# Kernel tuning notes

Hardware: AMD Instinct MI355X
Metric: run time of the kernel (lower is better)

The kernel has to match this reference:

```python
import jax, jax.numpy as jnp
import numpy as np

B, N, D, H = 8, 1024, 512, 512  # batch, nodes/graph, input dim, hidden/output dim
NEG_SLOPE = 0.2


def _gatv2_layer(x, src, dst, Wl, bl, Wr, br, a, bias, nseg):
    """PyG GATv2Conv (heads=1, add_self_loops=False, eval mode -> no dropout).
    message j->i: alpha_ij = softmax_i( a . leaky_relu(xl[j] + xr[i]) ); out[i] = sum_j alpha_ij * xl[j] + bias
    """
    xl = x @ Wl + bl              # [nseg, H] source transform
    xr = x @ Wr + br              # [nseg, H] target transform
    e = jax.nn.leaky_relu(xl[src] + xr[dst], NEG_SLOPE) @ a  # [E] raw scores
    m = jax.lax.stop_gradient(jax.ops.segment_max(e, dst, num_segments=nseg))
    ex = jnp.exp(e - m[dst])
    s = jax.ops.segment_sum(ex, dst, num_segments=nseg)
    alpha = ex / s[dst]                                       # segment softmax over incoming edges
    out = jax.ops.segment_sum(alpha[:, None] * xl[src], dst, num_segments=nseg)
    return out + bias


def setup_inputs() -> dict:
    key = jax.random.key(0)
    rng = np.random.RandomState(0)
    # random per-graph adjacency, avg degree ~16; block-diagonal edge extraction
    adj_np = (rng.rand(B, N, N) < (16.0 / N))
    srcs, dsts = [], []
    for b in range(B):  # matches torch.nonzero(big_adj).t(): row=src, col=dst
        r, c = np.nonzero(adj_np[b])
        srcs.append(r + b * N)
        dsts.append(c + b * N)
    edge_index = jnp.asarray(np.stack([np.concatenate(srcs), np.concatenate(dsts)]).astype(np.int32))

    ks = jax.random.split(key, 32)
    def lin(k, fi, fo):
        return (jax.random.normal(k, (fi, fo), jnp.float32) / np.sqrt(fi)).astype(jnp.float32)
    inp = {
        "batch_graph": jax.random.normal(ks[0], (B, N, D), jnp.float32),
        "adj": jnp.asarray(adj_np.astype(np.float32)),
        "edge_index": edge_index,
    }
    dims = [(D, H), (H, H), (H, H)]
    for i, (fi, fo) in enumerate(dims, start=1):
        k = jax.random.split(ks[i], 6)
        inp[f"Wl{i}"] = lin(k[0], fi, fo)
        inp[f"bl{i}"] = jnp.zeros((fo,), jnp.float32)
        inp[f"Wr{i}"] = lin(k[1], fi, fo)
        inp[f"br{i}"] = jnp.zeros((fo,), jnp.float32)
        inp[f"a{i}"] = (jax.random.normal(k[2], (fo,), jnp.float32) / np.sqrt(fo)).astype(jnp.float32)
        inp[f"bias{i}"] = jnp.zeros((fo,), jnp.float32)
    return inp


def reference(batch_graph, adj, edge_index,
              Wl1, bl1, Wr1, br1, a1, bias1,
              Wl2, bl2, Wr2, br2, a2, bias2,
              Wl3, bl3, Wr3, br3, a3, bias3):
    b, n, d = batch_graph.shape
    nseg = b * n
    x = batch_graph.reshape(nseg, d)
    src, dst = edge_index[0], edge_index[1]
    x = _gatv2_layer(x, src, dst, Wl1, bl1, Wr1, br1, a1, bias1, nseg)  # graph_norm = Identity
    x = _gatv2_layer(x, src, dst, Wl2, bl2, Wr2, br2, a2, bias2, nseg)
    x = _gatv2_layer(x, src, dst, Wl3, bl3, Wr3, br3, a3, bias3, nseg)
    return x.reshape(b, n, -1)
```

## Files before the change

kernel.cpp:

```cpp
#include <hip/hip_runtime.h>
#include <math.h>

#define MTOT 8192
#define HD   512

typedef __attribute__((ext_vector_type(8))) short bf16x8;
typedef __attribute__((ext_vector_type(4))) float floatx4;

__device__ inline unsigned short f2bf(float f) {
    unsigned int u = __float_as_uint(f);
    unsigned int r = (u + 0x7FFFu + ((u >> 16) & 1u)) >> 16;
    return (unsigned short)r;
}
__device__ inline float bf2f(unsigned short h) {
    return __uint_as_float(((unsigned int)h) << 16);
}


__global__ void count_deg(const int* __restrict__ dst, int* __restrict__ deg, int E) {
    int i = blockIdx.x * 256 + threadIdx.x;
    if (i < E) atomicAdd(&deg[dst[i]], 1);
}

__global__ __launch_bounds__(1024) void scan_offsets(const int* __restrict__ deg,
                                                     int* __restrict__ offs,
                                                     int* __restrict__ cursor) {
    __shared__ int part[1024];
    int tid = threadIdx.x;
    int base = tid * 8;
    int v[8]; int s = 0;
    #pragma unroll
    for (int i = 0; i < 8; ++i) { v[i] = deg[base + i]; s += v[i]; }
    part[tid] = s;
    __syncthreads();
    for (int off = 1; off < 1024; off <<= 1) {
        int t = (tid >= off) ? part[tid - off] : 0;
        __syncthreads();
        part[tid] += t;
        __syncthreads();
    }
    int run = (tid == 0) ? 0 : part[tid - 1];
    #pragma unroll
    for (int i = 0; i < 8; ++i) {
        offs[base + i] = run;
        cursor[base + i] = run;
        run += v[i];
    }
    if (tid == 1023) offs[MTOT] = run;
}

__global__ void scatter_edges(const int* __restrict__ src, const int* __restrict__ dst,
                              int* __restrict__ cursor, int* __restrict__ csr_src, int E) {
    int i = blockIdx.x * 256 + threadIdx.x;
    if (i < E) {
        int p = atomicAdd(&cursor[dst[i]], 1);
        csr_src[p] = src[i];
    }
}


__global__ __launch_bounds__(256) void prep_convert(
    const float* __restrict__ W0, const float* __restrict__ W1,
    const float* __restrict__ W2, const float* __restrict__ W3,
    const float* __restrict__ W4, const float* __restrict__ W5,
    unsigned short* __restrict__ wtbase,
    const float* __restrict__ X,
    unsigned short* __restrict__ Ahi, unsigned short* __restrict__ Alo,
    int* __restrict__ deg)
{
    int z = blockIdx.z;
    if (z == 7) {
        if (blockIdx.x == 0 && blockIdx.y == 0)
            for (int i = threadIdx.x; i < MTOT; i += 256) deg[i] = 0;
        return;
    }
    if (z == 6) {
        int bid = blockIdx.x * 16 + blockIdx.y;
        int t0 = bid * 256 + threadIdx.x;
        #pragma unroll
        for (int it = 0; it < 16; ++it) {
            int i = (t0 + it * 65536) * 4;
            float4 vv = *(const float4*)(X + i);
            ushort4 h, l;
            h.x = f2bf(vv.x); l.x = f2bf(vv.x - bf2f(h.x));
            h.y = f2bf(vv.y); l.y = f2bf(vv.y - bf2f(h.y));
            h.z = f2bf(vv.z); l.z = f2bf(vv.z - bf2f(h.z));
            h.w = f2bf(vv.w); l.w = f2bf(vv.w - bf2f(h.w));
            *(ushort4*)(Ahi + i) = h;
            *(ushort4*)(Alo + i) = l;
        }
        return;
    }
    const float* W = (z == 0) ? W0 : (z == 1) ? W1 : (z == 2) ? W2
                   : (z == 3) ? W3 : (z == 4) ? W4 : W5;
    int L = z >> 1, lr = z & 1;
    const size_t SZ = (size_t)HD * HD;
    unsigned short* Whi = wtbase + (L * 4 + lr * 2) * SZ;
    unsigned short* Wlo = Whi + SZ;

    __shared__ float t[32][33];
    int bx = blockIdx.x * 32;
    int by = blockIdx.y * 32;
    int tx = threadIdx.x & 31, ty = threadIdx.x >> 5;
    for (int i = ty; i < 32; i += 8)
        t[i][tx] = W[(size_t)(by + i) * HD + bx + tx];
    __syncthreads();
    for (int i = ty; i < 32; i += 8) {
        float vv = t[tx][i];
        unsigned short h = f2bf(vv);
        unsigned short l = f2bf(vv - bf2f(h));
        Whi[(size_t)(bx + i) * HD + by + tx] = h;
        Wlo[(size_t)(bx + i) * HD + by + tx] = l;
    }
}


__global__ __launch_bounds__(256) void gemm_mfma_dual(
    const unsigned short* __restrict__ Ahi, const unsigned short* __restrict__ Alo,
    const unsigned short* __restrict__ Bhi_l, const unsigned short* __restrict__ Blo_l,
    const unsigned short* __restrict__ Bhi_r, const unsigned short* __restrict__ Blo_r,
    const float* __restrict__ bias_l, const float* __restrict__ bias_r,
    float* __restrict__ Cl, float* __restrict__ Cr)
{
    const unsigned short* Bhi = blockIdx.z ? Bhi_r : Bhi_l;
    const unsigned short* Blo = blockIdx.z ? Blo_r : Blo_l;
    const float* bias         = blockIdx.z ? bias_r : bias_l;
    float* C                  = blockIdx.z ? Cr : Cl;

    __shared__ __align__(16) unsigned short lds[4 * 128 * 32];

    int tid = threadIdx.x;
    int wave = tid >> 6, lane = tid & 63;
    int bm = blockIdx.y * 128, bn = blockIdx.x * 128;

    const unsigned short* gsrc[4] = {Ahi, Alo, Bhi, Blo};
    int rowbase[4] = {bm, bm, bn, bn};

    const unsigned short* gbase =
        gsrc[wave] + (size_t)(rowbase[wave] + (lane >> 2)) * 512 + (lane & 3) * 8;

    floatx4 acc[4][4] = {};

    int wm = wave & 1, wn = wave >> 1;
    int lr = lane & 15, lq = lane >> 4;

    for (int k0 = 0; k0 < 512; k0 += 32) {
        const unsigned short* g = gbase + k0;
        #pragma unroll
        for (int rg = 0; rg < 8; ++rg) {
            __builtin_amdgcn_global_load_lds(
                (const __attribute__((address_space(1))) unsigned int*)(g + (size_t)rg * 16 * 512),
                (__attribute__((address_space(3))) unsigned int*)(&lds[wave * 4096 + rg * 512]),
                16, 0, 0);
        }
        __syncthreads();

        bf16x8 ah[4], al[4], bh[4], bl_[4];
        #pragma unroll
        for (int i = 0; i < 4; ++i) {
            int mrow = wm * 64 + i * 16 + lr;
            ah[i]  = *(const bf16x8*)&lds[0 * 4096 + mrow * 32 + lq * 8];
            al[i]  = *(const bf16x8*)&lds[1 * 4096 + mrow * 32 + lq * 8];
            int nrow = wn * 64 + i * 16 + lr;
            bh[i]  = *(const bf16x8*)&lds[2 * 4096 + nrow * 32 + lq * 8];
            bl_[i] = *(const bf16x8*)&lds[3 * 4096 + nrow * 32 + lq * 8];
        }
        #pragma unroll
        for (int i = 0; i < 4; ++i)
            #pragma unroll
            for (int j = 0; j < 4; ++j) {
                acc[i][j] = __builtin_amdgcn_mfma_f32_16x16x32_bf16(ah[i], bh[j],  acc[i][j], 0, 0, 0);
                acc[i][j] = __builtin_amdgcn_mfma_f32_16x16x32_bf16(ah[i], bl_[j], acc[i][j], 0, 0, 0);
                acc[i][j] = __builtin_amdgcn_mfma_f32_16x16x32_bf16(al[i], bh[j],  acc[i][j], 0, 0, 0);
            }
        __syncthreads();
    }

    #pragma unroll
    for (int j = 0; j < 4; ++j) {
        int n = bn + wn * 64 + j * 16 + lr;
        float bv = bias[n];
        #pragma unroll
        for (int i = 0; i < 4; ++i) {
            int mbase = bm + wm * 64 + i * 16 + lq * 4;
            #pragma unroll
            for (int r = 0; r < 4; ++r)
                C[(size_t)(mbase + r) * 512 + n] = acc[i][j][r] + bv;
        }
    }
}


__global__ __launch_bounds__(512) void gat_fused3(
    const float* __restrict__ xl, const float* __restrict__ xr,
    const float* __restrict__ avec, const float* __restrict__ bias,
    const int* __restrict__ offs, const int* __restrict__ csr_src,
    float* __restrict__ out, unsigned short* __restrict__ Ohi,
    unsigned short* __restrict__ Olo, int write_fp32)
{
    __shared__ float xr_sh[4][512];
    __shared__ float sc_sh[4][128];
    __shared__ int   idx_sh[4][128];
    __shared__ float inv_sh[4];

    int gid = blockIdx.x;
    int nbase = ((gid & 7) << 10) + ((gid >> 3) << 2);
    int tid = threadIdx.x;
    int wv = tid >> 6, lane = tid & 63;

    int o0 = offs[nbase], o1 = offs[nbase + 1], o2 = offs[nbase + 2];
    int o3 = offs[nbase + 3], o4 = offs[nbase + 4];

    {
        int row = tid >> 7, col = tid & 127;
        *(float4*)&xr_sh[row][col * 4] =
            *(const float4*)(xr + (size_t)(nbase + row) * HD + col * 4);
    }
    if (wv < 4) {
        int nb = (wv == 0) ? o0 : (wv == 1) ? o1 : (wv == 2) ? o2 : o3;
        int ne = (wv == 0) ? o1 : (wv == 1) ? o2 : (wv == 2) ? o3 : o4;
        int dg = ne - nb; if (dg > 128) dg = 128;
        for (int i = lane; i < dg; i += 64) idx_sh[wv][i] = csr_src[nb + i];
    }
    __syncthreads();

    {
        int sub = lane >> 4, flane = lane & 15;
        float4 av[8];
        #pragma unroll
        for (int i = 0; i < 8; ++i)
            av[i] = *(const float4*)(avec + i * 64 + flane * 4);

        for (int p0 = o0 + wv * 4; p0 < o4; p0 += 32) {
            int p = p0 + sub;
            bool valid = p < o4;
            int pc = valid ? p : o0;
            int nid = (pc >= o1) + (pc >= o2) + (pc >= o3);
            int nb = (nid == 0) ? o0 : (nid == 1) ? o1 : (nid == 2) ? o2 : o3;
            int local = pc - nb;
            valid = valid && (local < 128);
            int j = idx_sh[nid][valid ? local : 0];
            const float* xls = xl + (size_t)j * HD;
            float pe0 = 0.f, pe1 = 0.f;
            #pragma unroll
            for (int i = 0; i < 8; ++i) {
                float4 xv = *(const float4*)(xls + i * 64 + flane * 4);
                float4 rv = *(const float4*)&xr_sh[nid][i * 64 + flane * 4];
                float t;
                t = xv.x + rv.x; pe0 = fmaf(av[i].x, t, pe0); pe1 = fmaf(av[i].x, fabsf(t), pe1);
                t = xv.y + rv.y; pe0 = fmaf(av[i].y, t, pe0); pe1 = fmaf(av[i].y, fabsf(t), pe1);
                t = xv.z + rv.z; pe0 = fmaf(av[i].z, t, pe0); pe1 = fmaf(av[i].z, fabsf(t), pe1);
                t = xv.w + rv.w; pe0 = fmaf(av[i].w, t, pe0); pe1 = fmaf(av[i].w, fabsf(t), pe1);
            }
            float pe = fmaf(0.6f, pe0, 0.4f * pe1);
            pe += __shfl_xor(pe, 1, 64);
            pe += __shfl_xor(pe, 2, 64);
            pe += __shfl_xor(pe, 4, 64);
            pe += __shfl_xor(pe, 8, 64);
            if (valid && flane == 0) sc_sh[nid][local] = pe;
        }
    }
    __syncthreads();

    if (wv < 4) {
        int nb = (wv == 0) ? o0 : (wv == 1) ? o1 : (wv == 2) ? o2 : o3;
        int ne = (wv == 0) ? o1 : (wv == 1) ? o2 : (wv == 2) ? o3 : o4;
        int dg = ne - nb; if (dg > 128) dg = 128;
        float s0v = (lane < dg) ? sc_sh[wv][lane] : -1e30f;
        float s1v = (lane + 64 < dg) ? sc_sh[wv][lane + 64] : -1e30f;
        float m = fmaxf(s0v, s1v);
        #pragma unroll
        for (int off = 32; off; off >>= 1) m = fmaxf(m, __shfl_xor(m, off, 64));
        float e0 = (lane < dg) ? __expf(s0v - m) : 0.f;
        float e1 = (lane + 64 < dg) ? __expf(s1v - m) : 0.f;
        if (lane < dg) sc_sh[wv][lane] = e0;
        if (lane + 64 < dg) sc_sh[wv][lane + 64] = e1;
        float s = e0 + e1;
        #pragma unroll
        for (int off = 32; off; off >>= 1) s += __shfl_xor(s, off, 64);
        if (lane == 0) inv_sh[wv] = (s > 0.f) ? 1.f / s : 0.f;
    }
    __syncthreads();

    int nid = wv & 3, half = wv >> 2;
    int node = nbase + nid;
    int nb = (nid == 0) ? o0 : (nid == 1) ? o1 : (nid == 2) ? o2 : o3;
    int ne = (nid == 0) ? o1 : (nid == 1) ? o2 : (nid == 2) ? o3 : o4;
    int dg = ne - nb; if (dg > 128) dg = 128;
    int hb = half * 256 + lane * 4;

    float4 acc = {0.f, 0.f, 0.f, 0.f};
    int p = 0;
    for (; p + 8 <= dg; p += 8) {
        float w[8]; const float* q[8];
        #pragma unroll
        for (int u = 0; u < 8; ++u) {
            w[u] = sc_sh[nid][p + u];
            q[u] = xl + (size_t)idx_sh[nid][p + u] * HD + hb;
        }
        float4 x[8];
        #pragma unroll
        for (int u = 0; u < 8; ++u) x[u] = *(const float4*)q[u];
        #pragma unroll
        for (int u = 0; u < 8; ++u) {
            acc.x += w[u] * x[u].x; acc.y += w[u] * x[u].y;
            acc.z += w[u] * x[u].z; acc.w += w[u] * x[u].w;
        }
    }
    for (; p < dg; ++p) {
        float w = sc_sh[nid][p];
        const float* q = xl + (size_t)idx_sh[nid][p] * HD + hb;
        float4 x = *(const float4*)q;
        acc.x += w * x.x; acc.y += w * x.y; acc.z += w * x.z; acc.w += w * x.w;
    }

    float inv = inv_sh[nid];
    float4 bv = *(const float4*)(bias + hb);
    float4 o = {acc.x * inv + bv.x, acc.y * inv + bv.y,
                acc.z * inv + bv.z, acc.w * inv + bv.w};

    if (write_fp32) {
        *(float4*)(out + (size_t)node * HD + hb) = o;
    } else {
        size_t rb = (size_t)node * HD + hb;
        ushort4 h, lo;
        h.x = f2bf(o.x); lo.x = f2bf(o.x - bf2f(h.x));
        h.y = f2bf(o.y); lo.y = f2bf(o.y - bf2f(h.y));
        h.z = f2bf(o.z); lo.z = f2bf(o.z - bf2f(h.z));
        h.w = f2bf(o.w); lo.w = f2bf(o.w - bf2f(h.w));
        *(ushort4*)(Ohi + rb) = h;
        *(ushort4*)(Olo + rb) = lo;
    }
}


extern "C" void kernel_launch(void* const* d_in, const int* in_sizes, int n_in,
                              void* d_out, int out_size, void* d_ws, size_t ws_size,
                              hipStream_t stream) {
    const float* x0 = (const float*)d_in[0];
    const int* eidx = (const int*)d_in[2];
    int E = in_sizes[2] / 2;
    const int* esrc = eidx;
    const int* edst = eidx + E;

    const float* Wl[3] = {(const float*)d_in[3],  (const float*)d_in[9],  (const float*)d_in[15]};
    const float* bl[3] = {(const float*)d_in[4],  (const float*)d_in[10], (const float*)d_in[16]};
    const float* Wr[3] = {(const float*)d_in[5],  (const float*)d_in[11], (const float*)d_in[17]};
    const float* br[3] = {(const float*)d_in[6],  (const float*)d_in[12], (const float*)d_in[18]};
    const float* av[3] = {(const float*)d_in[7],  (const float*)d_in[13], (const float*)d_in[19]};
    const float* bs[3] = {(const float*)d_in[8],  (const float*)d_in[14], (const float*)d_in[20]};

    char* w = (char*)d_ws;
    unsigned short* Ahi = (unsigned short*)w; w += (size_t)MTOT * HD * 2;
    unsigned short* Alo = (unsigned short*)w; w += (size_t)MTOT * HD * 2;
    unsigned short* wtbase = (unsigned short*)w; w += 12 * (size_t)HD * HD * 2;
    float* xl = (float*)w; w += (size_t)MTOT * HD * 4;
    float* xr = (float*)w; w += (size_t)MTOT * HD * 4;
    int* deg    = (int*)w;
    int* offs   = deg + MTOT;
    int* cursor = offs + MTOT + 8;
    int* csr    = cursor + MTOT;
    const size_t SZ = (size_t)HD * HD;

    prep_convert<<<dim3(16, 16, 8), 256, 0, stream>>>(
        Wl[0], Wr[0], Wl[1], Wr[1], Wl[2], Wr[2], wtbase, x0, Ahi, Alo, deg);
    count_deg<<<(E + 255) / 256, 256, 0, stream>>>(edst, deg, E);
    scan_offsets<<<1, 1024, 0, stream>>>(deg, offs, cursor);
    scatter_edges<<<(E + 255) / 256, 256, 0, stream>>>(esrc, edst, cursor, csr, E);

    dim3 ggrid(HD / 128, MTOT / 128, 2);
    for (int L = 0; L < 3; ++L) {
        gemm_mfma_dual<<<ggrid, 256, 0, stream>>>(Ahi, Alo,
            wtbase + (L * 4 + 0) * SZ, wtbase + (L * 4 + 1) * SZ,
            wtbase + (L * 4 + 2) * SZ, wtbase + (L * 4 + 3) * SZ,
            bl[L], br[L], xl, xr);
        int last = (L == 2);
        gat_fused3<<<MTOT / 4, 512, 0, stream>>>(xl, xr, av[L], bs[L], offs, csr,
                                                 last ? (float*)d_out : nullptr,
                                                 last ? nullptr : Ahi,
                                                 last ? nullptr : Alo,
                                                 last);
    }
}
```

Measured before the change: 337.9 us.

## Fuse a·xl/a·xr projections into GEMM epilogue and use online-softmax GAT aggregation

The GEMM epilogue now also computes per-row partial dot products of xl and xr with the attention vector and writes them to small workspace arrays. This relies on the identity leaky_relu(t) = 0.6t + 0.4|t|, so the linear part of the score comes from those precomputed partials. The GAT kernel is replaced by a one-wave-per-node online-softmax loop. Each edge's xl row is read once, serving both the |t| score term and the weighted accumulation, with the next row prefetched. This removes the second gather of xl rows, the shared-memory staging and the 128-degree cap. In exchange it serializes edges per wave, adds a full-wave reduction per edge, and adds extra shuffles in the GEMM epilogue.

```diff
diff --git a/kernel.cpp b/kernel.cpp
--- a/kernel.cpp
+++ b/kernel.cpp
@@ -120,12 +120,15 @@
     const unsigned short* __restrict__ Bhi_l, const unsigned short* __restrict__ Blo_l,
     const unsigned short* __restrict__ Bhi_r, const unsigned short* __restrict__ Blo_r,
     const float* __restrict__ bias_l, const float* __restrict__ bias_r,
-    float* __restrict__ Cl, float* __restrict__ Cr)
+    float* __restrict__ Cl, float* __restrict__ Cr,
+    const float* __restrict__ avec,
+    float* __restrict__ slpart, float* __restrict__ srpart)
 {
     const unsigned short* Bhi = blockIdx.z ? Bhi_r : Bhi_l;
     const unsigned short* Blo = blockIdx.z ? Blo_r : Blo_l;
     const float* bias         = blockIdx.z ? bias_r : bias_l;
     float* C                  = blockIdx.z ? Cr : Cl;
+    float* spart              = blockIdx.z ? srpart : slpart;
 
     __shared__ __align__(16) unsigned short lds[4 * 128 * 32];
 
@@ -188,148 +191,160 @@
                 C[(size_t)(mbase + r) * 512 + n] = acc[i][j][r] + bv;
         }
     }
-}
-
-
-__global__ __launch_bounds__(512) void gat_fused3(
+
+    {
+        float aj[4], bj[4];
+        #pragma unroll
+        for (int j = 0; j < 4; ++j) {
+            int n = bn + wn * 64 + j * 16 + lr;
+            aj[j] = avec[n];
+            bj[j] = bias[n];
+        }
+        float badd = fmaf(aj[0], bj[0], fmaf(aj[1], bj[1],
+                     fmaf(aj[2], bj[2], aj[3] * bj[3])));
+        #pragma unroll
+        for (int i = 0; i < 4; ++i) {
+            #pragma unroll
+            for (int r = 0; r < 4; ++r) {
+                float v = fmaf(aj[0], acc[i][0][r],
+                          fmaf(aj[1], acc[i][1][r],
+                          fmaf(aj[2], acc[i][2][r],
+                          fmaf(aj[3], acc[i][3][r], badd))));
+                v += __shfl_xor(v, 1, 64);
+                v += __shfl_xor(v, 2, 64);
+                v += __shfl_xor(v, 4, 64);
+                v += __shfl_xor(v, 8, 64);
+                if (lr == 0) {
+                    int row = bm + wm * 64 + i * 16 + lq * 4 + r;
+                    spart[(size_t)row * 8 + blockIdx.x * 2 + wn] = v;
+                }
+            }
+        }
+    }
+}
+
+
+__global__ __launch_bounds__(256) void gat_online(
     const float* __restrict__ xl, const float* __restrict__ xr,
+    const float* __restrict__ slpart, const float* __restrict__ srpart,
     const float* __restrict__ avec, const float* __restrict__ bias,
     const int* __restrict__ offs, const int* __restrict__ csr_src,
     float* __restrict__ out, unsigned short* __restrict__ Ohi,
     unsigned short* __restrict__ Olo, int write_fp32)
 {
-    __shared__ float xr_sh[4][512];
-    __shared__ float sc_sh[4][128];
-    __shared__ int   idx_sh[4][128];
-    __shared__ float inv_sh[4];
-
     int gid = blockIdx.x;
-    int nbase = ((gid & 7) << 10) + ((gid >> 3) << 2);
-    int tid = threadIdx.x;
-    int wv = tid >> 6, lane = tid & 63;
-
-    int o0 = offs[nbase], o1 = offs[nbase + 1], o2 = offs[nbase + 2];
-    int o3 = offs[nbase + 3], o4 = offs[nbase + 4];
-
-    {
-        int row = tid >> 7, col = tid & 127;
-        *(float4*)&xr_sh[row][col * 4] =
-            *(const float4*)(xr + (size_t)(nbase + row) * HD + col * 4);
-    }
-    if (wv < 4) {
-        int nb = (wv == 0) ? o0 : (wv == 1) ? o1 : (wv == 2) ? o2 : o3;
-        int ne = (wv == 0) ? o1 : (wv == 1) ? o2 : (wv == 2) ? o3 : o4;
-        int dg = ne - nb; if (dg > 128) dg = 128;
-        for (int i = lane; i < dg; i += 64) idx_sh[wv][i] = csr_src[nb + i];
-    }
-    __syncthreads();
-
-    {
-        int sub = lane >> 4, flane = lane & 15;
-        float4 av[8];
-        #pragma unroll
-        for (int i = 0; i < 8; ++i)
-            av[i] = *(const float4*)(avec + i * 64 + flane * 4);
-
-        for (int p0 = o0 + wv * 4; p0 < o4; p0 += 32) {
-            int p = p0 + sub;
-            bool valid = p < o4;
-            int pc = valid ? p : o0;
-            int nid = (pc >= o1) + (pc >= o2) + (pc >= o3);
-            int nb = (nid == 0) ? o0 : (nid == 1) ? o1 : (nid == 2) ? o2 : o3;
-            int local = pc - nb;
-            valid = valid && (local < 128);
-            int j = idx_sh[nid][valid ? local : 0];
-            const float* xls = xl + (size_t)j * HD;
-            float pe0 = 0.f, pe1 = 0.f;
-            #pragma unroll
-            for (int i = 0; i < 8; ++i) {
-                float4 xv = *(const float4*)(xls + i * 64 + flane * 4);
-                float4 rv = *(const float4*)&xr_sh[nid][i * 64 + flane * 4];
-                float t;
-                t = xv.x + rv.x; pe0 = fmaf(av[i].x, t, pe0); pe1 = fmaf(av[i].x, fabsf(t), pe1);
-                t = xv.y + rv.y; pe0 = fmaf(av[i].y, t, pe0); pe1 = fmaf(av[i].y, fabsf(t), pe1);
-                t = xv.z + rv.z; pe0 = fmaf(av[i].z, t, pe0); pe1 = fmaf(av[i].z, fabsf(t), pe1);
-                t = xv.w + rv.w; pe0 = fmaf(av[i].w, t, pe0); pe1 = fmaf(av[i].w, fabsf(t), pe1);
-            }
-            float pe = fmaf(0.6f, pe0, 0.4f * pe1);
-            pe += __shfl_xor(pe, 1, 64);
-            pe += __shfl_xor(pe, 2, 64);
-            pe += __shfl_xor(pe, 4, 64);
-            pe += __shfl_xor(pe, 8, 64);
-            if (valid && flane == 0) sc_sh[nid][local] = pe;
-        }
-    }
-    __syncthreads();
-
-    if (wv < 4) {
-        int nb = (wv == 0) ? o0 : (wv == 1) ? o1 : (wv == 2) ? o2 : o3;
-        int ne = (wv == 0) ? o1 : (wv == 1) ? o2 : (wv == 2) ? o3 : o4;
-        int dg = ne - nb; if (dg > 128) dg = 128;
-        float s0v = (lane < dg) ? sc_sh[wv][lane] : -1e30f;
-        float s1v = (lane + 64 < dg) ? sc_sh[wv][lane + 64] : -1e30f;
-        float m = fmaxf(s0v, s1v);
-        #pragma unroll
-        for (int off = 32; off; off >>= 1) m = fmaxf(m, __shfl_xor(m, off, 64));
-        float e0 = (lane < dg) ? __expf(s0v - m) : 0.f;
-        float e1 = (lane + 64 < dg) ? __expf(s1v - m) : 0.f;
-        if (lane < dg) sc_sh[wv][lane] = e0;
-        if (lane + 64 < dg) sc_sh[wv][lane + 64] = e1;
-        float s = e0 + e1;
-        #pragma unroll
-        for (int off = 32; off; off >>= 1) s += __shfl_xor(s, off, 64);
-        if (lane == 0) inv_sh[wv] = (s > 0.f) ? 1.f / s : 0.f;
-    }
-    __syncthreads();
-
-    int nid = wv & 3, half = wv >> 2;
-    int node = nbase + nid;
-    int nb = (nid == 0) ? o0 : (nid == 1) ? o1 : (nid == 2) ? o2 : o3;
-    int ne = (nid == 0) ? o1 : (nid == 1) ? o2 : (nid == 2) ? o3 : o4;
-    int dg = ne - nb; if (dg > 128) dg = 128;
-    int hb = half * 256 + lane * 4;
-
-    float4 acc = {0.f, 0.f, 0.f, 0.f};
-    int p = 0;
-    for (; p + 8 <= dg; p += 8) {
-        float w[8]; const float* q[8];
-        #pragma unroll
-        for (int u = 0; u < 8; ++u) {
-            w[u] = sc_sh[nid][p + u];
-            q[u] = xl + (size_t)idx_sh[nid][p + u] * HD + hb;
-        }
-        float4 x[8];
-        #pragma unroll
-        for (int u = 0; u < 8; ++u) x[u] = *(const float4*)q[u];
-        #pragma unroll
-        for (int u = 0; u < 8; ++u) {
-            acc.x += w[u] * x[u].x; acc.y += w[u] * x[u].y;
-            acc.z += w[u] * x[u].z; acc.w += w[u] * x[u].w;
-        }
-    }
-    for (; p < dg; ++p) {
-        float w = sc_sh[nid][p];
-        const float* q = xl + (size_t)idx_sh[nid][p] * HD + hb;
-        float4 x = *(const float4*)q;
-        acc.x += w * x.x; acc.y += w * x.y; acc.z += w * x.z; acc.w += w * x.w;
-    }
-
-    float inv = inv_sh[nid];
-    float4 bv = *(const float4*)(bias + hb);
-    float4 o = {acc.x * inv + bv.x, acc.y * inv + bv.y,
-                acc.z * inv + bv.z, acc.w * inv + bv.w};
+    int wv = threadIdx.x >> 6, lane = threadIdx.x & 63;
+    int node = ((gid & 7) << 10) + ((gid >> 3) << 2) + wv;
+
+    int nb = offs[node], ne = offs[node + 1];
+
+    size_t rowoff = (size_t)node * HD + lane * 8;
+    float4 r0 = *(const float4*)(xr + rowoff);
+    float4 r1 = *(const float4*)(xr + rowoff + 4);
+    float4 av0 = *(const float4*)(avec + lane * 8);
+    float4 av1 = *(const float4*)(avec + lane * 8 + 4);
+
+    float4 sr0 = *(const float4*)(srpart + (size_t)node * 8);
+    float4 sr1 = *(const float4*)(srpart + (size_t)node * 8 + 4);
+    float sr = ((sr0.x + sr0.y) + (sr0.z + sr0.w)) + ((sr1.x + sr1.y) + (sr1.z + sr1.w));
+
+    float m = -3.0e38f, s = 0.f;
+    float4 acc0 = {0.f, 0.f, 0.f, 0.f}, acc1 = {0.f, 0.f, 0.f, 0.f};
+
+    int p = nb;
+    int jnx = 0;
+    float4 nx0 = {0,0,0,0}, nx1 = {0,0,0,0}, nsl0 = {0,0,0,0}, nsl1 = {0,0,0,0};
+    if (p < ne) {
+        int j0 = __builtin_amdgcn_readfirstlane(csr_src[p]);
+        const float* xp = xl + (size_t)j0 * HD + lane * 8;
+        nx0 = *(const float4*)xp;
+        nx1 = *(const float4*)(xp + 4);
+        nsl0 = *(const float4*)(slpart + (size_t)j0 * 8);
+        nsl1 = *(const float4*)(slpart + (size_t)j0 * 8 + 4);
+    }
+    if (p + 1 < ne) jnx = __builtin_amdgcn_readfirstlane(csr_src[p + 1]);
+
+    while (p < ne) {
+        float4 cx0 = nx0, cx1 = nx1;
+        float slj = ((nsl0.x + nsl0.y) + (nsl0.z + nsl0.w)) +
+                    ((nsl1.x + nsl1.y) + (nsl1.z + nsl1.w));
+
+        int jpre = jnx;
+        if (p + 2 < ne) jnx = __builtin_amdgcn_readfirstlane(csr_src[p + 2]);
+        if (p + 1 < ne) {
+            const float* xp = xl + (size_t)jpre * HD + lane * 8;
+            nx0 = *(const float4*)xp;
+            nx1 = *(const float4*)(xp + 4);
+            nsl0 = *(const float4*)(slpart + (size_t)jpre * 8);
+            nsl1 = *(const float4*)(slpart + (size_t)jpre * 8 + 4);
+        }
+
+        float t, pe = 0.f;
+        t = cx0.x + r0.x; pe = fmaf(av0.x, fabsf(t), pe);
+        t = cx0.y + r0.y; pe = fmaf(av0.y, fabsf(t), pe);
+        t = cx0.z + r0.z; pe = fmaf(av0.z, fabsf(t), pe);
+        t = cx0.w + r0.w; pe = fmaf(av0.w, fabsf(t), pe);
+        t = cx1.x + r1.x; pe = fmaf(av1.x, fabsf(t), pe);
+        t = cx1.y + r1.y; pe = fmaf(av1.y, fabsf(t), pe);
+        t = cx1.z + r1.z; pe = fmaf(av1.z, fabsf(t), pe);
+        t = cx1.w + r1.w; pe = fmaf(av1.w, fabsf(t), pe);
+        pe += __shfl_xor(pe, 1, 64);
+        pe += __shfl_xor(pe, 2, 64);
+        pe += __shfl_xor(pe, 4, 64);
+        pe += __shfl_xor(pe, 8, 64);
+        pe += __shfl_xor(pe, 16, 64);
+        pe += __shfl_xor(pe, 32, 64);
+
+        float e = fmaf(0.4f, pe, 0.6f * (slj + sr));
+
+        float w;
+        if (e > m) {
+            float sc = __expf(m - e);
+            s *= sc;
+            acc0.x *= sc; acc0.y *= sc; acc0.z *= sc; acc0.w *= sc;
+            acc1.x *= sc; acc1.y *= sc; acc1.z *= sc; acc1.w *= sc;
+            m = e; w = 1.f;
+        } else {
+            w = __expf(e - m);
+        }
+        s += w;
+        acc0.x = fmaf(w, cx0.x, acc0.x);
+        acc0.y = fmaf(w, cx0.y, acc0.y);
+        acc0.z = fmaf(w, cx0.z, acc0.z);
+        acc0.w = fmaf(w, cx0.w, acc0.w);
+        acc1.x = fmaf(w, cx1.x, acc1.x);
+        acc1.y = fmaf(w, cx1.y, acc1.y);
+        acc1.z = fmaf(w, cx1.z, acc1.z);
+        acc1.w = fmaf(w, cx1.w, acc1.w);
+        ++p;
+    }
+
+    float inv = (s > 0.f) ? 1.f / s : 0.f;
+    float4 b0 = *(const float4*)(bias + lane * 8);
+    float4 b1 = *(const float4*)(bias + lane * 8 + 4);
+    float4 o0, o1;
+    o0.x = fmaf(acc0.x, inv, b0.x); o0.y = fmaf(acc0.y, inv, b0.y);
+    o0.z = fmaf(acc0.z, inv, b0.z); o0.w = fmaf(acc0.w, inv, b0.w);
+    o1.x = fmaf(acc1.x, inv, b1.x); o1.y = fmaf(acc1.y, inv, b1.y);
+    o1.z = fmaf(acc1.z, inv, b1.z); o1.w = fmaf(acc1.w, inv, b1.w);
 
     if (write_fp32) {
-        *(float4*)(out + (size_t)node * HD + hb) = o;
+        *(float4*)(out + rowoff) = o0;
+        *(float4*)(out + rowoff + 4) = o1;
     } else {
-        size_t rb = (size_t)node * HD + hb;
         ushort4 h, lo;
-        h.x = f2bf(o.x); lo.x = f2bf(o.x - bf2f(h.x));
-        h.y = f2bf(o.y); lo.y = f2bf(o.y - bf2f(h.y));
-        h.z = f2bf(o.z); lo.z = f2bf(o.z - bf2f(h.z));
-        h.w = f2bf(o.w); lo.w = f2bf(o.w - bf2f(h.w));
-        *(ushort4*)(Ohi + rb) = h;
-        *(ushort4*)(Olo + rb) = lo;
+        h.x = f2bf(o0.x); lo.x = f2bf(o0.x - bf2f(h.x));
+        h.y = f2bf(o0.y); lo.y = f2bf(o0.y - bf2f(h.y));
+        h.z = f2bf(o0.z); lo.z = f2bf(o0.z - bf2f(h.z));
+        h.w = f2bf(o0.w); lo.w = f2bf(o0.w - bf2f(h.w));
+        *(ushort4*)(Ohi + rowoff) = h;
+        *(ushort4*)(Olo + rowoff) = lo;
+        h.x = f2bf(o1.x); lo.x = f2bf(o1.x - bf2f(h.x));
+        h.y = f2bf(o1.y); lo.y = f2bf(o1.y - bf2f(h.y));
+        h.z = f2bf(o1.z); lo.z = f2bf(o1.z - bf2f(h.z));
+        h.w = f2bf(o1.w); lo.w = f2bf(o1.w - bf2f(h.w));
+        *(ushort4*)(Ohi + rowoff + 4) = h;
+        *(ushort4*)(Olo + rowoff + 4) = lo;
     }
 }
 
@@ -360,6 +375,8 @@
     int* offs   = deg + MTOT;
     int* cursor = offs + MTOT + 8;
     int* csr    = cursor + MTOT;
+    float* slpart = (float*)(((uintptr_t)(csr + E) + 63) & ~(uintptr_t)63);
+    float* srpart = slpart + (size_t)MTOT * 8;
     const size_t SZ = (size_t)HD * HD;
 
     prep_convert<<<dim3(16, 16, 8), 256, 0, stream>>>(
@@ -373,9 +390,10 @@
         gemm_mfma_dual<<<ggrid, 256, 0, stream>>>(Ahi, Alo,
             wtbase + (L * 4 + 0) * SZ, wtbase + (L * 4 + 1) * SZ,
             wtbase + (L * 4 + 2) * SZ, wtbase + (L * 4 + 3) * SZ,
-            bl[L], br[L], xl, xr);
+            bl[L], br[L], xl, xr, av[L], slpart, srpart);
         int last = (L == 2);
-        gat_fused3<<<MTOT / 4, 512, 0, stream>>>(xl, xr, av[L], bs[L], offs, csr,
+        gat_online<<<MTOT / 4, 256, 0, stream>>>(xl, xr, slpart, srpart, av[L], bs[L],
+                                                 offs, csr,
                                                  last ? (float*)d_out : nullptr,
                                                  last ? nullptr : Ahi,
                                                  last ? nullptr : Alo,
```

New measurement: 346.6 us. 1.03x slower.
